# Performance work log

Hardware: AMD Instinct MI355X
Metric: run time of the kernel (lower is better)

Reference implementation:

```python
import jax, jax.numpy as jnp
import numpy as np

N, E, IN_DIM, HID = 50000, 800000, 128, 64
NEG_SLOPE = 0.01  # torch F.leaky_relu default


def setup_inputs() -> dict:
    key = jax.random.key(0)
    ks = jax.random.split(key, 8)
    x = jax.random.normal(ks[0], (N, IN_DIM), jnp.float32)
    edge_index = jax.random.randint(ks[1], (2, E), 0, N, dtype=jnp.int32)
    edge_weight = jax.random.uniform(ks[2], (E,), jnp.float32)
    h = jnp.zeros((N, HID), jnp.float32)
    c = jnp.zeros((N, HID), jnp.float32)
    sx = 1.0 / np.sqrt(IN_DIM)
    sh = 1.0 / np.sqrt(HID)
    # gate order along leading axis: [i, f, c(tilde), o]; K=2 Chebyshev weights
    Wx = (jax.random.normal(ks[3], (4, 2, IN_DIM, HID), jnp.float32) * sx)
    bx = jnp.zeros((4, HID), jnp.float32)
    Wh = (jax.random.normal(ks[4], (4, 2, HID, HID), jnp.float32) * sh)
    bh = jnp.zeros((4, HID), jnp.float32)
    wc = jax.random.normal(ks[5], (3, HID), jnp.float32) * 0.1  # peepholes for i, f, o
    bg = jnp.zeros((4, HID), jnp.float32)
    W_head = jax.random.normal(ks[6], (HID, 1), jnp.float32) * sh
    b_head = jnp.zeros((1,), jnp.float32)
    return dict(x=x, edge_index=edge_index, edge_weight=edge_weight, h=h, c=c,
                Wx=Wx, bx=bx, Wh=Wh, bh=bh, wc=wc, bg=bg, W_head=W_head, b_head=b_head)


def _cheb_norm(src, dst, ew, n):
    # ChebConv 'sym' normalization with lambda_max=2: L_hat = -D^{-1/2} A D^{-1/2}
    # (the +1 self-loop from the Laplacian cancels against fill_value=-1)
    deg = jnp.zeros((n,), ew.dtype).at[src].add(ew)
    dinv = jnp.where(deg > 0, 1.0 / jnp.sqrt(jnp.where(deg > 0, deg, 1.0)), 0.0)
    return -dinv[src] * ew * dinv[dst]


def _prop(feat, src, dst, norm, n):
    # T1 = L_hat @ feat via edge gather + segment-sum
    return jax.ops.segment_sum(norm[:, None] * feat[src], dst, num_segments=n)


def reference(x, edge_index, edge_weight, h, c, Wx, bx, Wh, bh, wc, bg, W_head, b_head):
    n = x.shape[0]
    src, dst = edge_index[0], edge_index[1]
    norm = _cheb_norm(src, dst, edge_weight, n)
    Tx = _prop(x, src, dst, norm, n)
    Th = _prop(h, src, dst, norm, n)  # shared across all 4 h-side ChebConvs
    # z[g] = X W[g,0] + (L_hat X) W[g,1] + b  for all gates at once
    z = (jnp.einsum('nd,gdh->gnh', x, Wx[:, 0]) + jnp.einsum('nd,gdh->gnh', Tx, Wx[:, 1]) + bx[:, None, :]
         + jnp.einsum('nd,gdh->gnh', h, Wh[:, 0]) + jnp.einsum('nd,gdh->gnh', Th, Wh[:, 1]) + bh[:, None, :])
    i = jax.nn.sigmoid(z[0] + wc[0] * c + bg[0])
    f = jax.nn.sigmoid(z[1] + wc[1] * c + bg[1])
    g = jnp.tanh(z[2] + bg[2])
    c_new = f * c + i * g
    o = jax.nn.sigmoid(z[3] + wc[2] * c_new + bg[3])
    h_new = o * jnp.tanh(c_new)
    out = jax.nn.leaky_relu(h_new, NEG_SLOPE) @ W_head + b_head
    return out, h_new, c_new
```

## Files before the change

kernel.cpp:

```cpp
#include <hip/hip_runtime.h>
#include <hip/hip_bf16.h>

#define IN_DIM 128
#define HID 64
#define NEG_SLOPE 0.01f
#define CAP 5120

typedef __attribute__((ext_vector_type(8))) short short8;
typedef __attribute__((ext_vector_type(4))) short short4v;
typedef __attribute__((ext_vector_type(4))) float f32x4;
typedef unsigned short ushort_t;
typedef unsigned int uint_t;

__device__ __forceinline__ float fsig(float x) { return 1.f / (1.f + __expf(-x)); }
__device__ __forceinline__ float ftanh(float x) { return 1.f - 2.f / (__expf(2.f * x) + 1.f); }

__device__ __forceinline__ ushort_t f2bf(float f) {
    uint_t u = __float_as_uint(f);
    uint_t r = u + 0x7fffu + ((u >> 16) & 1u);
    return (ushort_t)(r >> 16);
}
__device__ __forceinline__ float bf2f(ushort_t s) { return __uint_as_float(((uint_t)s) << 16); }
__device__ __forceinline__ float bf2f_s(short s) { return bf2f((ushort_t)s); }

__global__ __launch_bounds__(256) void part_kernel(
    const int* __restrict__ src, const int* __restrict__ dst, const float* __restrict__ ew,
    const float* __restrict__ x, const float* __restrict__ h,
    const float* __restrict__ Wx, const float* __restrict__ Wh,
    int* __restrict__ cur_d, int* __restrict__ cur_s,
    int2* __restrict__ dpart, int2* __restrict__ spart,
    uint_t* __restrict__ xb_u, uint_t* __restrict__ hb_u, ushort_t* __restrict__ Wp,
    int E, int N, int nbPart) {
    __shared__ int hd[256], hs[256];
    int t = threadIdx.x;

    if ((int)blockIdx.x < nbPart) {
        hd[t] = 0; hs[t] = 0;
        __syncthreads();
        int base = blockIdx.x * 2048;
        int sv[8], dv[8]; float wv[8];
#pragma unroll
        for (int it = 0; it < 8; ++it) {
            int e = base + it * 256 + t;
            bool ok = e < E;
            sv[it] = ok ? src[e] : 0;
            dv[it] = ok ? dst[e] : 0;
            wv[it] = ok ? ew[e] : 0.f;
            if (ok) {
                atomicAdd(&hd[dv[it] >> 8], 1);
                atomicAdd(&hs[sv[it] >> 8], 1);
            }
        }
        __syncthreads();
        int nd = hd[t], ns = hs[t];
        __syncthreads();
        if (nd) hd[t] = atomicAdd(&cur_d[t * 16], nd);
        if (ns) hs[t] = atomicAdd(&cur_s[t * 16], ns);
        __syncthreads();
#pragma unroll
        for (int it = 0; it < 8; ++it) {
            int e = base + it * 256 + t;
            if (e < E) {
                int d = dv[it], s = sv[it];
                int bd = d >> 8, bs = s >> 8;
                int pd = atomicAdd(&hd[bd], 1);
                int ps = atomicAdd(&hs[bs], 1);
                dpart[(size_t)bd * CAP + pd] = make_int2(s | ((d & 255) << 16), __float_as_int(wv[it]));
                spart[(size_t)bs * CAP + ps] = make_int2(s & 255, __float_as_int(wv[it]));
            }
        }
        return;
    }

    int cb = blockIdx.x - nbPart;
    int tid = cb * 256 + t;
    int T = (gridDim.x - nbPart) * 256;
    int ncvt = N * 96;
    int nx = N * 64;
    for (int i = tid; i < ncvt; i += T) {
        if (i < nx) {
            float2 v = ((const float2*)x)[i];
            xb_u[i] = (uint_t)f2bf(v.x) | ((uint_t)f2bf(v.y) << 16);
        } else {
            int j = i - nx;
            float2 v = ((const float2*)h)[j];
            hb_u[j] = (uint_t)f2bf(v.x) | ((uint_t)f2bf(v.y) << 16);
        }
    }

    for (int idx = tid; idx < 384 * 256; idx += T) {
        int j = idx & 7;
        int tmp = idx >> 3;
        int lane = tmp & 63;
        int t2 = tmp >> 6;
        int ct = t2 & 15;
        int ks = t2 >> 4;
        int k = ks * 32 + (lane >> 4) * 8 + j;
        int colg = ct * 16 + (lane & 15);
        int g = colg >> 6, hdd = colg & 63;
        float v;
        if (k < 128)      v = Wx[((g * 2 + 0) * 128 + k) * 64 + hdd];
        else if (k < 192) v = Wh[((g * 2 + 0) * 64 + (k - 128)) * 64 + hdd];
        else if (k < 320) v = Wx[((g * 2 + 1) * 128 + (k - 192)) * 64 + hdd];
        else              v = Wh[((g * 2 + 1) * 64 + (k - 320)) * 64 + hdd];
        Wp[idx] = f2bf(v);
    }
}

__global__ __launch_bounds__(256) void deg_kernel(const int2* __restrict__ spart,
                                                  const int* __restrict__ cur_s,
                                                  float* __restrict__ dinv, int N) {
    __shared__ float df[256];
    int t = threadIdx.x, b = blockIdx.x;
    df[t] = 0.f;
    __syncthreads();
    int cnt = cur_s[b * 16];
    for (int i = t; i < cnt; i += 256) {
        int2 r = spart[(size_t)b * CAP + i];
        atomicAdd(&df[r.x & 255], __int_as_float(r.y));
    }
    __syncthreads();
    int g = b * 256 + t;
    if (g < N) {
        float dd = df[t];
        dinv[g] = dd > 0.f ? rsqrtf(dd) : 0.f;
    }
}

__global__ __launch_bounds__(256) void fillb_kernel(const int2* __restrict__ dpart,
                                                    const int* __restrict__ cur_d,
                                                    const float* __restrict__ dinv,
                                                    int* __restrict__ rowptr, int* __restrict__ rowend,
                                                    int2* __restrict__ eprm, int N) {
    __shared__ int c[256], sdata[256], pcur[256];
    __shared__ float dl[256];
    int t = threadIdx.x, b = blockIdx.x;
    c[t] = 0;
    int g = b * 256 + t;
    dl[t] = (g < N) ? dinv[g] : 0.f;
    __syncthreads();
    int cnt = cur_d[b * 16];
    for (int i = t; i < cnt; i += 256) {
        int m = dpart[(size_t)b * CAP + i].x;
        atomicAdd(&c[(m >> 16) & 255], 1);
    }
    __syncthreads();
    sdata[t] = c[t];
    __syncthreads();
    for (int off = 1; off < 256; off <<= 1) {
        int tmp = (t >= off) ? sdata[t - off] : 0;
        __syncthreads();
        sdata[t] += tmp;
        __syncthreads();
    }
    int excl = sdata[t] - c[t];
    pcur[t] = excl;
    if (g < N) {
        rowptr[g] = b * CAP + excl;
        rowend[g] = b * CAP + sdata[t];
    }
    __syncthreads();
    for (int i = t; i < cnt; i += 256) {
        int2 r = dpart[(size_t)b * CAP + i];
        int m = r.x;
        int dlo = (m >> 16) & 255;
        int s = m & 0xffff;
        float w = __int_as_float(r.y);
        int pos = atomicAdd(&pcur[dlo], 1);
        float nrm = -dinv[s] * w * dl[dlo];
        eprm[(size_t)b * CAP + pos] = make_int2(s, __float_as_int(nrm));
    }
}

#define GQ_LOAD(SS, WW, XV, HV, QOFF)                                          \
    _Pragma("unroll")                                                          \
    for (int q = 0; q < 4; ++q) {                                              \
        SS[q] = __shfl(sv, sl0 + (QOFF) + q);                                  \
        WW[q] = __shfl(wv, sl0 + (QOFF) + q);                                  \
        XV[q] = *(const short8*)(xb + (size_t)SS[q] * 128 + l16 * 8);          \
        HV[q] = *(const short4v*)(hb + (size_t)SS[q] * 64 + l16 * 4);          \
    }

#define GQ_FMA(WW, XV, HV)                                                     \
    _Pragma("unroll")                                                          \
    for (int q = 0; q < 4; ++q) {                                              \
        _Pragma("unroll")                                                      \
        for (int i = 0; i < 8; ++i) ax[i] += WW[q] * bf2f_s(XV[q][i]);         \
        _Pragma("unroll")                                                      \
        for (int i = 0; i < 4; ++i) ah[i] += WW[q] * bf2f_s(HV[q][i]);         \
    }

__global__ __launch_bounds__(256) void gather_kernel(const int* __restrict__ rowptr,
                                                     const int* __restrict__ rowend,
                                                     const int2* __restrict__ eprm,
                                                     const ushort_t* __restrict__ xb,
                                                     const ushort_t* __restrict__ hb,
                                                     ushort_t* __restrict__ Txb,
                                                     ushort_t* __restrict__ Thb, int N) {
    int lane = threadIdx.x & 63;
    int wave = threadIdx.x >> 6;
    int grp = lane >> 4, l16 = lane & 15;
    int node = blockIdx.x * 16 + wave * 4 + grp;
    bool valid = node < N;
    int p = 0, end = 0;
    if (valid) { p = rowptr[node]; end = rowend[node]; }

    float ax[8] = {0.f, 0.f, 0.f, 0.f, 0.f, 0.f, 0.f, 0.f};
    float ah[4] = {0.f, 0.f, 0.f, 0.f};

    int idx0 = p + l16;
    int2 pr = (idx0 < end) ? eprm[idx0] : make_int2(0, 0);

    int sl0 = grp * 16;
    for (int base = p; base < end; base += 16) {
        int2 cur = pr;
        int nidx = base + 16 + l16;
        if (base + 16 < end) pr = (nidx < end) ? eprm[nidx] : make_int2(0, 0);
        int sv = cur.x;
        float wv = __int_as_float(cur.y);

        int sA[4]; float wA[4]; short8 xA[4]; short4v hA[4];
        int sB[4]; float wB[4]; short8 xB[4]; short4v hB[4];
        GQ_LOAD(sA, wA, xA, hA, 0)
        GQ_LOAD(sB, wB, xB, hB, 4)
        GQ_FMA(wA, xA, hA)
        GQ_LOAD(sA, wA, xA, hA, 8)
        GQ_FMA(wB, xB, hB)
        GQ_LOAD(sB, wB, xB, hB, 12)
        GQ_FMA(wA, xA, hA)
        GQ_FMA(wB, xB, hB)
    }

    if (valid) {
        short8 tx;
#pragma unroll
        for (int i = 0; i < 8; ++i) tx[i] = (short)f2bf(ax[i]);
        *(short8*)(Txb + (size_t)node * 128 + l16 * 8) = tx;
        short4v th;
#pragma unroll
        for (int i = 0; i < 4; ++i) th[i] = (short)f2bf(ah[i]);
        *(short4v*)(Thb + (size_t)node * 64 + l16 * 4) = th;
    }
}

__global__ __launch_bounds__(256, 4) void fused_mfma(
    const ushort_t* __restrict__ xb, const ushort_t* __restrict__ hb,
    const ushort_t* __restrict__ Txb, const ushort_t* __restrict__ Thb,
    const float* __restrict__ c_in, const ushort_t* __restrict__ Wp,
    const float* __restrict__ bx, const float* __restrict__ bh,
    const float* __restrict__ wc, const float* __restrict__ bg,
    const float* __restrict__ Whead, const float* __restrict__ bhead,
    float* __restrict__ out, int N) {
    __shared__ ushort_t Bs[2][8192];
    int tid = threadIdx.x;
    int lane = tid & 63;
    int wave = tid >> 6;
    int quad = lane >> 4, m = lane & 15;
    int row0 = (blockIdx.x * 4 + wave) * 16;
    int ar = row0 + m; if (ar >= N) ar = N - 1;
    int ko = quad * 8;

    {
        const float4* gsrc = (const float4*)(Wp);
        float4* ldst = (float4*)Bs[0];
#pragma unroll
        for (int i = 0; i < 4; ++i) ldst[tid + 256 * i] = gsrc[tid + 256 * i];
    }

    f32x4 acc[16];
#pragma unroll
    for (int ct = 0; ct < 16; ++ct) {
        int g = ct >> 2, hd = (ct & 3) * 16 + m;
        float b = bx[g * 64 + hd] + bh[g * 64 + hd];
        f32x4 bb = {b, b, b, b};
        acc[ct] = bb;
    }

    __syncthreads();

#pragma unroll
    for (int ks = 0; ks < 12; ++ks) {
        int buf = ks & 1;
        float4 tmp[4];
        if (ks < 11) {
            const float4* gsrc = (const float4*)(Wp + (ks + 1) * 8192);
#pragma unroll
            for (int i = 0; i < 4; ++i) tmp[i] = gsrc[tid + 256 * i];
        }
        const ushort_t* a;
        if (ks < 4)       a = xb  + (size_t)ar * 128 + ks * 32 + ko;
        else if (ks < 6)  a = hb  + (size_t)ar * 64 + (ks - 4) * 32 + ko;
        else if (ks < 10) a = Txb + (size_t)ar * 128 + (ks - 6) * 32 + ko;
        else              a = Thb + (size_t)ar * 64 + (ks - 10) * 32 + ko;
        short8 af = *(const short8*)a;
        const short8* bsp = (const short8*)Bs[buf];
#pragma unroll
        for (int ct = 0; ct < 16; ++ct) {
            short8 bf = bsp[ct * 64 + lane];
            acc[ct] = __builtin_amdgcn_mfma_f32_16x16x32_bf16(af, bf, acc[ct], 0, 0, 0);
        }
        if (ks < 11) {
            float4* ldst = (float4*)Bs[buf ^ 1];
#pragma unroll
            for (int i = 0; i < 4; ++i) ldst[tid + 256 * i] = tmp[i];
            __syncthreads();
        }
    }

    float hp[4] = {0.f, 0.f, 0.f, 0.f};
    float bhv = bhead[0];

#pragma unroll
    for (int hs = 0; hs < 4; ++hs) {
        int hd = hs * 16 + m;
        float wc0 = wc[hd], wc1 = wc[64 + hd], wc2 = wc[128 + hd];
        float bg0 = bg[hd], bg1 = bg[64 + hd], bg2 = bg[128 + hd], bg3 = bg[192 + hd];
        float wh = Whead[hd];
#pragma unroll
        for (int reg = 0; reg < 4; ++reg) {
            int n = row0 + quad * 4 + reg;
            if (n < N) {
                float c_old = c_in[(size_t)n * 64 + hd];
                float zi = acc[0 * 4 + hs][reg];
                float zf = acc[1 * 4 + hs][reg];
                float zg = acc[2 * 4 + hs][reg];
                float zo = acc[3 * 4 + hs][reg];
                float ii = fsig(zi + wc0 * c_old + bg0);
                float ff = fsig(zf + wc1 * c_old + bg1);
                float gg = ftanh(zg + bg2);
                float cn = ff * c_old + ii * gg;
                float oo = fsig(zo + wc2 * cn + bg3);
                float hn = oo * ftanh(cn);
                out[N + (size_t)n * 64 + hd] = hn;
                out[N + (size_t)N * 64 + (size_t)n * 64 + hd] = cn;
                float lr = hn > 0.f ? hn : NEG_SLOPE * hn;
                hp[reg] += lr * wh;
            }
        }
    }
#pragma unroll
    for (int reg = 0; reg < 4; ++reg) {
        float v0 = hp[reg];
#pragma unroll
        for (int mask = 1; mask < 16; mask <<= 1) v0 += __shfl_xor(v0, mask);
        if (m == 0) {
            int n0_ = row0 + quad * 4 + reg;
            if (n0_ < N) out[n0_] = v0 + bhv;
        }
    }
}

extern "C" void kernel_launch(void* const* d_in, const int* in_sizes, int n_in,
                              void* d_out, int out_size, void* d_ws, size_t ws_size,
                              hipStream_t stream) {
    const float* x = (const float*)d_in[0];
    const int* ei = (const int*)d_in[1];
    const float* ew = (const float*)d_in[2];
    const float* h = (const float*)d_in[3];
    const float* c = (const float*)d_in[4];
    const float* Wx = (const float*)d_in[5];
    const float* bx = (const float*)d_in[6];
    const float* Wh = (const float*)d_in[7];
    const float* bh = (const float*)d_in[8];
    const float* wc = (const float*)d_in[9];
    const float* bg = (const float*)d_in[10];
    const float* Whead = (const float*)d_in[11];
    const float* bhead = (const float*)d_in[12];

    int N = in_sizes[0] / IN_DIM;
    int E = in_sizes[1] / 2;
    const int* src = ei;
    const int* dst = ei + E;

    int nbuck = (N + 255) >> 8;
    int nbPart = (E + 2047) / 2048;

    char* wp = (char*)d_ws;
    auto alloc = [&](size_t bytes) {
        char* p = wp;
        wp += (bytes + 255) & ~(size_t)255;
        return p;
    };
    int* cur = (int*)alloc((size_t)2 * nbuck * 16 * 4);
    int* cur_d = cur;
    int* cur_s = cur + (size_t)nbuck * 16;
    float* dinv = (float*)alloc((size_t)N * 4);
    int* rowptr = (int*)alloc((size_t)N * 4);
    int* rowend = (int*)alloc((size_t)N * 4);
    int2* dpart = (int2*)alloc((size_t)nbuck * CAP * 8);
    int2* spart = (int2*)alloc((size_t)nbuck * CAP * 8);
    int2* eprm = spart;
    ushort_t* xb = (ushort_t*)alloc((size_t)N * 128 * 2);
    ushort_t* hb = (ushort_t*)alloc((size_t)N * 64 * 2);
    ushort_t* Txb = (ushort_t*)alloc((size_t)N * 128 * 2);
    ushort_t* Thb = (ushort_t*)alloc((size_t)N * 64 * 2);
    ushort_t* Wp = (ushort_t*)alloc((size_t)384 * 256 * 2);

    hipMemsetAsync(cur, 0, (size_t)2 * nbuck * 16 * 4, stream);

    part_kernel<<<2048, 256, 0, stream>>>(src, dst, ew, x, h, Wx, Wh,
                                          cur_d, cur_s, dpart, spart,
                                          (uint_t*)xb, (uint_t*)hb, Wp, E, N, nbPart);
    deg_kernel<<<nbuck, 256, 0, stream>>>(spart, cur_s, dinv, N);
    fillb_kernel<<<nbuck, 256, 0, stream>>>(dpart, cur_d, dinv, rowptr, rowend, eprm, N);
    gather_kernel<<<(N + 15) / 16, 256, 0, stream>>>(rowptr, rowend, eprm, xb, hb, Txb, Thb, N);
    fused_mfma<<<(N + 63) / 64, 256, 0, stream>>>(xb, hb, Txb, Thb, c, Wp, bx, bh, wc, bg,
                                                  Whead, bhead, (float*)d_out, N);
}
```

Baseline: 237.2 us.

## Merge pipeline stages into one cooperative persistent kernel with grid syncs

The five separate kernels and the memset (partition/convert, degree, CSR fill, gather, fused MFMA) become device functions. They are called in sequence from a single cooperative mega_kernel, with grid.sync barriers between phases and grid-stride loops over units and tiles. The goal is to remove per-launch gaps and the memset launch. The cost is that every phase now runs on a grid capped by occupancy, and each phase boundary pays for a grid-wide barrier. The old multi-kernel path stays as a fallback when the cooperative launch is unavailable or too small.

```diff
diff --git a/kernel.cpp b/kernel.cpp
--- a/kernel.cpp
+++ b/kernel.cpp
@@ -1,5 +1,8 @@
 #include <hip/hip_runtime.h>
+#include <hip/hip_cooperative_groups.h>
 #include <hip/hip_bf16.h>
+
+namespace cg = cooperative_groups;
 
 #define IN_DIM 128
 #define HID 64
@@ -23,58 +26,55 @@
 __device__ __forceinline__ float bf2f(ushort_t s) { return __uint_as_float(((uint_t)s) << 16); }
 __device__ __forceinline__ float bf2f_s(short s) { return bf2f((ushort_t)s); }
 
-__global__ __launch_bounds__(256) void part_kernel(
+struct PartShared { int hd[256]; int hs[256]; };
+struct FillShared { int c[256]; int sdata[256]; int pcur[256]; float dl[256]; };
+
+__device__ __forceinline__ void dev_part_chunk(
+    int pb, int t, PartShared& sm,
     const int* __restrict__ src, const int* __restrict__ dst, const float* __restrict__ ew,
+    int* __restrict__ cur_d, int* __restrict__ cur_s,
+    int2* __restrict__ dpart, int2* __restrict__ spart, int E) {
+    sm.hd[t] = 0; sm.hs[t] = 0;
+    __syncthreads();
+    int base = pb * 2048;
+    int sv[8], dv[8]; float wv[8];
+#pragma unroll
+    for (int it = 0; it < 8; ++it) {
+        int e = base + it * 256 + t;
+        bool ok = e < E;
+        sv[it] = ok ? src[e] : 0;
+        dv[it] = ok ? dst[e] : 0;
+        wv[it] = ok ? ew[e] : 0.f;
+        if (ok) {
+            atomicAdd(&sm.hd[dv[it] >> 8], 1);
+            atomicAdd(&sm.hs[sv[it] >> 8], 1);
+        }
+    }
+    __syncthreads();
+    int nd = sm.hd[t], ns = sm.hs[t];
+    __syncthreads();
+    if (nd) sm.hd[t] = atomicAdd(&cur_d[t * 16], nd);
+    if (ns) sm.hs[t] = atomicAdd(&cur_s[t * 16], ns);
+    __syncthreads();
+#pragma unroll
+    for (int it = 0; it < 8; ++it) {
+        int e = base + it * 256 + t;
+        if (e < E) {
+            int d = dv[it], s = sv[it];
+            int bd = d >> 8, bs = s >> 8;
+            int pd = atomicAdd(&sm.hd[bd], 1);
+            int ps = atomicAdd(&sm.hs[bs], 1);
+            dpart[(size_t)bd * CAP + pd] = make_int2(s | ((d & 255) << 16), __float_as_int(wv[it]));
+            spart[(size_t)bs * CAP + ps] = make_int2(s & 255, __float_as_int(wv[it]));
+        }
+    }
+}
+
+__device__ __forceinline__ void dev_cvt(
+    int tid, int T,
     const float* __restrict__ x, const float* __restrict__ h,
     const float* __restrict__ Wx, const float* __restrict__ Wh,
-    int* __restrict__ cur_d, int* __restrict__ cur_s,
-    int2* __restrict__ dpart, int2* __restrict__ spart,
-    uint_t* __restrict__ xb_u, uint_t* __restrict__ hb_u, ushort_t* __restrict__ Wp,
-    int E, int N, int nbPart) {
-    __shared__ int hd[256], hs[256];
-    int t = threadIdx.x;
-
-    if ((int)blockIdx.x < nbPart) {
-        hd[t] = 0; hs[t] = 0;
-        __syncthreads();
-        int base = blockIdx.x * 2048;
-        int sv[8], dv[8]; float wv[8];
-#pragma unroll
-        for (int it = 0; it < 8; ++it) {
-            int e = base + it * 256 + t;
-            bool ok = e < E;
-            sv[it] = ok ? src[e] : 0;
-            dv[it] = ok ? dst[e] : 0;
-            wv[it] = ok ? ew[e] : 0.f;
-            if (ok) {
-                atomicAdd(&hd[dv[it] >> 8], 1);
-                atomicAdd(&hs[sv[it] >> 8], 1);
-            }
-        }
-        __syncthreads();
-        int nd = hd[t], ns = hs[t];
-        __syncthreads();
-        if (nd) hd[t] = atomicAdd(&cur_d[t * 16], nd);
-        if (ns) hs[t] = atomicAdd(&cur_s[t * 16], ns);
-        __syncthreads();
-#pragma unroll
-        for (int it = 0; it < 8; ++it) {
-            int e = base + it * 256 + t;
-            if (e < E) {
-                int d = dv[it], s = sv[it];
-                int bd = d >> 8, bs = s >> 8;
-                int pd = atomicAdd(&hd[bd], 1);
-                int ps = atomicAdd(&hs[bs], 1);
-                dpart[(size_t)bd * CAP + pd] = make_int2(s | ((d & 255) << 16), __float_as_int(wv[it]));
-                spart[(size_t)bs * CAP + ps] = make_int2(s & 255, __float_as_int(wv[it]));
-            }
-        }
-        return;
-    }
-
-    int cb = blockIdx.x - nbPart;
-    int tid = cb * 256 + t;
-    int T = (gridDim.x - nbPart) * 256;
+    uint_t* __restrict__ xb_u, uint_t* __restrict__ hb_u, ushort_t* __restrict__ Wp, int N) {
     int ncvt = N * 96;
     int nx = N * 64;
     for (int i = tid; i < ncvt; i += T) {
@@ -87,7 +87,6 @@
             hb_u[j] = (uint_t)f2bf(v.x) | ((uint_t)f2bf(v.y) << 16);
         }
     }
-
     for (int idx = tid; idx < 384 * 256; idx += T) {
         int j = idx & 7;
         int tmp = idx >> 3;
@@ -107,11 +106,10 @@
     }
 }
 
-__global__ __launch_bounds__(256) void deg_kernel(const int2* __restrict__ spart,
-                                                  const int* __restrict__ cur_s,
-                                                  float* __restrict__ dinv, int N) {
-    __shared__ float df[256];
-    int t = threadIdx.x, b = blockIdx.x;
+__device__ __forceinline__ void dev_deg(
+    int b, int t, float* df,
+    const int2* __restrict__ spart, const int* __restrict__ cur_s,
+    float* __restrict__ dinv, int N) {
     df[t] = 0.f;
     __syncthreads();
     int cnt = cur_s[b * 16];
@@ -127,37 +125,34 @@
     }
 }
 
-__global__ __launch_bounds__(256) void fillb_kernel(const int2* __restrict__ dpart,
-                                                    const int* __restrict__ cur_d,
-                                                    const float* __restrict__ dinv,
-                                                    int* __restrict__ rowptr, int* __restrict__ rowend,
-                                                    int2* __restrict__ eprm, int N) {
-    __shared__ int c[256], sdata[256], pcur[256];
-    __shared__ float dl[256];
-    int t = threadIdx.x, b = blockIdx.x;
-    c[t] = 0;
+__device__ __forceinline__ void dev_fillb(
+    int b, int t, FillShared& sm,
+    const int2* __restrict__ dpart, const int* __restrict__ cur_d,
+    const float* __restrict__ dinv,
+    int* __restrict__ rowptr, int* __restrict__ rowend, int2* __restrict__ eprm, int N) {
+    sm.c[t] = 0;
     int g = b * 256 + t;
-    dl[t] = (g < N) ? dinv[g] : 0.f;
+    sm.dl[t] = (g < N) ? dinv[g] : 0.f;
     __syncthreads();
     int cnt = cur_d[b * 16];
     for (int i = t; i < cnt; i += 256) {
         int m = dpart[(size_t)b * CAP + i].x;
-        atomicAdd(&c[(m >> 16) & 255], 1);
-    }
-    __syncthreads();
-    sdata[t] = c[t];
+        atomicAdd(&sm.c[(m >> 16) & 255], 1);
+    }
+    __syncthreads();
+    sm.sdata[t] = sm.c[t];
     __syncthreads();
     for (int off = 1; off < 256; off <<= 1) {
-        int tmp = (t >= off) ? sdata[t - off] : 0;
+        int tmp = (t >= off) ? sm.sdata[t - off] : 0;
         __syncthreads();
-        sdata[t] += tmp;
+        sm.sdata[t] += tmp;
         __syncthreads();
     }
-    int excl = sdata[t] - c[t];
-    pcur[t] = excl;
+    int excl = sm.sdata[t] - sm.c[t];
+    sm.pcur[t] = excl;
     if (g < N) {
         rowptr[g] = b * CAP + excl;
-        rowend[g] = b * CAP + sdata[t];
+        rowend[g] = b * CAP + sm.sdata[t];
     }
     __syncthreads();
     for (int i = t; i < cnt; i += 256) {
@@ -166,8 +161,8 @@
         int dlo = (m >> 16) & 255;
         int s = m & 0xffff;
         float w = __int_as_float(r.y);
-        int pos = atomicAdd(&pcur[dlo], 1);
-        float nrm = -dinv[s] * w * dl[dlo];
+        int pos = atomicAdd(&sm.pcur[dlo], 1);
+        float nrm = -dinv[s] * w * sm.dl[dlo];
         eprm[(size_t)b * CAP + pos] = make_int2(s, __float_as_int(nrm));
     }
 }
@@ -190,17 +185,14 @@
         for (int i = 0; i < 4; ++i) ah[i] += WW[q] * bf2f_s(HV[q][i]);         \
     }
 
-__global__ __launch_bounds__(256) void gather_kernel(const int* __restrict__ rowptr,
-                                                     const int* __restrict__ rowend,
-                                                     const int2* __restrict__ eprm,
-                                                     const ushort_t* __restrict__ xb,
-                                                     const ushort_t* __restrict__ hb,
-                                                     ushort_t* __restrict__ Txb,
-                                                     ushort_t* __restrict__ Thb, int N) {
-    int lane = threadIdx.x & 63;
-    int wave = threadIdx.x >> 6;
+__device__ __forceinline__ void dev_gather_unit(
+    int unit, int lane,
+    const int* __restrict__ rowptr, const int* __restrict__ rowend,
+    const int2* __restrict__ eprm,
+    const ushort_t* __restrict__ xb, const ushort_t* __restrict__ hb,
+    ushort_t* __restrict__ Txb, ushort_t* __restrict__ Thb, int N) {
     int grp = lane >> 4, l16 = lane & 15;
-    int node = blockIdx.x * 16 + wave * 4 + grp;
+    int node = unit * 4 + grp;
     bool valid = node < N;
     int p = 0, end = 0;
     if (valid) { p = rowptr[node]; end = rowend[node]; }
@@ -243,7 +235,8 @@
     }
 }
 
-__global__ __launch_bounds__(256, 4) void fused_mfma(
+__device__ __forceinline__ void dev_fused_tile(
+    int tile, int tid, ushort_t (*Bs)[8192],
     const ushort_t* __restrict__ xb, const ushort_t* __restrict__ hb,
     const ushort_t* __restrict__ Txb, const ushort_t* __restrict__ Thb,
     const float* __restrict__ c_in, const ushort_t* __restrict__ Wp,
@@ -251,12 +244,10 @@
     const float* __restrict__ wc, const float* __restrict__ bg,
     const float* __restrict__ Whead, const float* __restrict__ bhead,
     float* __restrict__ out, int N) {
-    __shared__ ushort_t Bs[2][8192];
-    int tid = threadIdx.x;
     int lane = tid & 63;
     int wave = tid >> 6;
     int quad = lane >> 4, m = lane & 15;
-    int row0 = (blockIdx.x * 4 + wave) * 16;
+    int row0 = (tile * 4 + wave) * 16;
     int ar = row0 + m; if (ar >= N) ar = N - 1;
     int ko = quad * 8;
 
@@ -348,6 +339,131 @@
             if (n0_ < N) out[n0_] = v0 + bhv;
         }
     }
+}
+
+__global__ __launch_bounds__(256, 4) void mega_kernel(
+    const int* __restrict__ src, const int* __restrict__ dst, const float* __restrict__ ew,
+    const float* __restrict__ x, const float* __restrict__ h,
+    const float* __restrict__ Wx, const float* __restrict__ Wh,
+    int* __restrict__ cur_d, int* __restrict__ cur_s,
+    int2* __restrict__ dpart, int2* __restrict__ spart,
+    ushort_t* __restrict__ xb, ushort_t* __restrict__ hb,
+    ushort_t* __restrict__ Txb, ushort_t* __restrict__ Thb,
+    ushort_t* __restrict__ Wp,
+    float* __restrict__ dinv, int* __restrict__ rowptr, int* __restrict__ rowend,
+    int2* __restrict__ eprm,
+    const float* __restrict__ c_in, const float* __restrict__ bx, const float* __restrict__ bh,
+    const float* __restrict__ wc, const float* __restrict__ bg,
+    const float* __restrict__ Whead, const float* __restrict__ bhead,
+    float* __restrict__ out,
+    int E, int N, int nbPart, int nbuck) {
+    __shared__ union {
+        PartShared part;
+        float df[256];
+        FillShared fill;
+        ushort_t Bs[2][8192];
+    } su;
+    cg::grid_group grid = cg::this_grid();
+    int t = threadIdx.x;
+    int bid = blockIdx.x;
+    int nb = gridDim.x;
+
+    for (int i = bid * 256 + t; i < 2 * nbuck * 16; i += nb * 256) cur_d[i] = 0;
+    __threadfence();
+    grid.sync();
+
+    if (bid < nbPart) {
+        dev_part_chunk(bid, t, su.part, src, dst, ew, cur_d, cur_s, dpart, spart, E);
+    } else {
+        int cb = bid - nbPart;
+        dev_cvt(cb * 256 + t, (nb - nbPart) * 256, x, h, Wx, Wh,
+                (uint_t*)xb, (uint_t*)hb, Wp, N);
+    }
+    __threadfence();
+    grid.sync();
+
+    if (bid < nbuck) dev_deg(bid, t, su.df, spart, cur_s, dinv, N);
+    __threadfence();
+    grid.sync();
+
+    if (bid < nbuck) dev_fillb(bid, t, su.fill, dpart, cur_d, dinv, rowptr, rowend, eprm, N);
+    __threadfence();
+    grid.sync();
+
+    {
+        int lane = t & 63, wave = t >> 6;
+        int nunits = (N + 3) >> 2;
+        for (int u = bid * 4 + wave; u < nunits; u += nb * 4)
+            dev_gather_unit(u, lane, rowptr, rowend, eprm, xb, hb, Txb, Thb, N);
+    }
+    __threadfence();
+    grid.sync();
+
+    {
+        int ntiles = (N + 63) >> 6;
+        for (int tile = bid; tile < ntiles; tile += nb)
+            dev_fused_tile(tile, t, su.Bs, xb, hb, Txb, Thb, c_in, Wp,
+                           bx, bh, wc, bg, Whead, bhead, out, N);
+    }
+}
+
+__global__ __launch_bounds__(256) void part_kernel(
+    const int* __restrict__ src, const int* __restrict__ dst, const float* __restrict__ ew,
+    const float* __restrict__ x, const float* __restrict__ h,
+    const float* __restrict__ Wx, const float* __restrict__ Wh,
+    int* __restrict__ cur_d, int* __restrict__ cur_s,
+    int2* __restrict__ dpart, int2* __restrict__ spart,
+    uint_t* __restrict__ xb_u, uint_t* __restrict__ hb_u, ushort_t* __restrict__ Wp,
+    int E, int N, int nbPart) {
+    __shared__ PartShared sm;
+    int t = threadIdx.x;
+    if ((int)blockIdx.x < nbPart) {
+        dev_part_chunk(blockIdx.x, t, sm, src, dst, ew, cur_d, cur_s, dpart, spart, E);
+        return;
+    }
+    int cb = blockIdx.x - nbPart;
+    dev_cvt(cb * 256 + t, (gridDim.x - nbPart) * 256, x, h, Wx, Wh, xb_u, hb_u, Wp, N);
+}
+
+__global__ __launch_bounds__(256) void deg_kernel(const int2* __restrict__ spart,
+                                                  const int* __restrict__ cur_s,
+                                                  float* __restrict__ dinv, int N) {
+    __shared__ float df[256];
+    dev_deg(blockIdx.x, threadIdx.x, df, spart, cur_s, dinv, N);
+}
+
+__global__ __launch_bounds__(256) void fillb_kernel(const int2* __restrict__ dpart,
+                                                    const int* __restrict__ cur_d,
+                                                    const float* __restrict__ dinv,
+                                                    int* __restrict__ rowptr, int* __restrict__ rowend,
+                                                    int2* __restrict__ eprm, int N) {
+    __shared__ FillShared sm;
+    dev_fillb(blockIdx.x, threadIdx.x, sm, dpart, cur_d, dinv, rowptr, rowend, eprm, N);
+}
+
+__global__ __launch_bounds__(256) void gather_kernel(const int* __restrict__ rowptr,
+                                                     const int* __restrict__ rowend,
+                                                     const int2* __restrict__ eprm,
+                                                     const ushort_t* __restrict__ xb,
+                                                     const ushort_t* __restrict__ hb,
+                                                     ushort_t* __restrict__ Txb,
+                                                     ushort_t* __restrict__ Thb, int N) {
+    int lane = threadIdx.x & 63;
+    int wave = threadIdx.x >> 6;
+    dev_gather_unit(blockIdx.x * 4 + wave, lane, rowptr, rowend, eprm, xb, hb, Txb, Thb, N);
+}
+
+__global__ __launch_bounds__(256, 4) void fused_mfma(
+    const ushort_t* __restrict__ xb, const ushort_t* __restrict__ hb,
+    const ushort_t* __restrict__ Txb, const ushort_t* __restrict__ Thb,
+    const float* __restrict__ c_in, const ushort_t* __restrict__ Wp,
+    const float* __restrict__ bx, const float* __restrict__ bh,
+    const float* __restrict__ wc, const float* __restrict__ bg,
+    const float* __restrict__ Whead, const float* __restrict__ bhead,
+    float* __restrict__ out, int N) {
+    __shared__ ushort_t Bs[2][8192];
+    dev_fused_tile(blockIdx.x, threadIdx.x, Bs, xb, hb, Txb, Thb, c_in, Wp,
+                   bx, bh, wc, bg, Whead, bhead, out, N);
 }
 
 extern "C" void kernel_launch(void* const* d_in, const int* in_sizes, int n_in,
@@ -396,8 +512,30 @@
     ushort_t* Thb = (ushort_t*)alloc((size_t)N * 64 * 2);
     ushort_t* Wp = (ushort_t*)alloc((size_t)384 * 256 * 2);
 
+    float* outp = (float*)d_out;
+
+    int maxPerCU = 0;
+    hipError_t qerr = hipOccupancyMaxActiveBlocksPerMultiprocessor(&maxPerCU, mega_kernel, 256, 0);
+    int coopGrid = (qerr == hipSuccess) ? maxPerCU * 256 : 0;
+    if (coopGrid > 1024) coopGrid = 1024;
+
+    if (coopGrid >= 512) {
+        void* args[] = {
+            (void*)&src, (void*)&dst, (void*)&ew, (void*)&x, (void*)&h,
+            (void*)&Wx, (void*)&Wh, (void*)&cur_d, (void*)&cur_s,
+            (void*)&dpart, (void*)&spart, (void*)&xb, (void*)&hb,
+            (void*)&Txb, (void*)&Thb, (void*)&Wp, (void*)&dinv,
+            (void*)&rowptr, (void*)&rowend, (void*)&eprm, (void*)&c,
+            (void*)&bx, (void*)&bh, (void*)&wc, (void*)&bg,
+            (void*)&Whead, (void*)&bhead, (void*)&outp,
+            (void*)&E, (void*)&N, (void*)&nbPart, (void*)&nbuck};
+        hipError_t lerr = hipLaunchCooperativeKernel((const void*)mega_kernel,
+                                                     dim3(coopGrid), dim3(256),
+                                                     args, 0, stream);
+        if (lerr == hipSuccess) return;
+    }
+
     hipMemsetAsync(cur, 0, (size_t)2 * nbuck * 16 * 4, stream);
-
     part_kernel<<<2048, 256, 0, stream>>>(src, dst, ew, x, h, Wx, Wh,
                                           cur_d, cur_s, dpart, spart,
                                           (uint_t*)xb, (uint_t*)hb, Wp, E, N, nbPart);
@@ -405,5 +543,5 @@
     fillb_kernel<<<nbuck, 256, 0, stream>>>(dpart, cur_d, dinv, rowptr, rowend, eprm, N);
     gather_kernel<<<(N + 15) / 16, 256, 0, stream>>>(rowptr, rowend, eprm, xb, hb, Txb, Thb, N);
     fused_mfma<<<(N + 63) / 64, 256, 0, stream>>>(xb, hb, Txb, Thb, c, Wp, bx, bh, wc, bg,
-                                                  Whead, bhead, (float*)d_out, N);
-}
+                                                  Whead, bhead, outp, N);
+}
```

After: 920.3 us. 288% more time.
